# Performance work log

Measured on AMD Instinct MI355X. Metric: run time of the kernel, lower is better.

The kernel has to match this reference:

```python
import jax, jax.numpy as jnp
import numpy as np

N = 10000        # nodes
E = 160000       # edges (before self-loops)
NFEAT = 256
NHID = 128
H = 4            # heads
NCLASS = 40
NLAYERS = 2
DT = 1.0
ALPHA = 1.0
GAMMA = 1.0
NEG_SLOPE = 0.2  # GATConv leaky_relu slope


def setup_inputs() -> dict:
    key = jax.random.key(0)
    ks = jax.random.split(key, 12)

    def glorot(k, shape):
        fan_in, fan_out = shape[-1], shape[0]
        lim = (6.0 / (fan_in + fan_out)) ** 0.5
        return jax.random.uniform(k, shape, jnp.float32, -lim, lim)

    return {
        "x": jax.random.normal(ks[0], (N, NFEAT), jnp.float32),
        "edge_index": jax.random.randint(ks[1], (2, E), 0, N, jnp.int64),
        "enc_w": glorot(ks[2], (NHID, NFEAT)),
        "enc_b": jnp.zeros((NHID,), jnp.float32),
        "res_w": glorot(ks[3], (H * NHID, NHID)),
        "res_b": jnp.zeros((H * NHID,), jnp.float32),
        "gat_w": glorot(ks[4], (H * NHID, NHID)),
        "att_src": glorot(ks[5], (H, NHID)) * 0.1,
        "att_dst": glorot(ks[6], (H, NHID)) * 0.1,
        "gat_b": jnp.zeros((H * NHID,), jnp.float32),
        "dec_w": glorot(ks[7], (NCLASS, NHID)),
        "dec_b": jnp.zeros((NCLASS,), jnp.float32),
    }


def _gat_conv(x, src, dst, gat_w, att_src, att_dst, gat_b):
    # x: [N, NHID] -> per-head features [N, H, C]
    xh = (x @ gat_w.T).reshape(N, H, NHID)
    a_src = jnp.sum(xh * att_src[None], axis=-1)  # [N, H]
    a_dst = jnp.sum(xh * att_dst[None], axis=-1)  # [N, H]
    e = jax.nn.leaky_relu(a_src[src] + a_dst[dst], NEG_SLOPE)  # [E', H]
    # segment softmax over incoming edges of each destination node
    m = jax.ops.segment_max(e, dst, num_segments=N)            # [N, H]
    e = jnp.exp(e - m[dst])
    s = jax.ops.segment_sum(e, dst, num_segments=N)            # [N, H]
    alpha = e / s[dst]                                          # [E', H]
    msg = xh[src] * alpha[:, :, None]                           # [E', H, C]
    out = jax.ops.segment_sum(msg, dst, num_segments=N)         # [N, H, C]
    return out.reshape(N, H * NHID) + gat_b


def reference(x, edge_index, enc_w, enc_b, res_w, res_b, gat_w,
              att_src, att_dst, gat_b, dec_w, dec_b):
    # add self-loops (GATConv default)
    loop = jnp.arange(N, dtype=edge_index.dtype)
    src = jnp.concatenate([edge_index[0], loop])
    dst = jnp.concatenate([edge_index[1], loop])

    Y = jax.nn.relu(x @ enc_w.T + enc_b)  # [N, NHID]
    X = Y
    for _ in range(NLAYERS):
        conv = _gat_conv(X, src, dst, gat_w, att_src, att_dst, gat_b)  # [N, H*NHID]
        res = X @ res_w.T + res_b                                       # [N, H*NHID]
        # faithful to .view(n_nodes, -1, nheads).mean(-1): [N, NHID, H] -> mean over heads axis
        z = jax.nn.elu(conv + res).reshape(N, NHID, H).mean(axis=-1)    # [N, NHID]
        Y = Y + DT * (z - ALPHA * Y - GAMMA * X)
        X = X + DT * Y
    return X @ dec_w.T + dec_b  # [N, NCLASS]
```

## Files before the change

kernel.cpp:

```cpp
#include <hip/hip_runtime.h>
#include <math.h>

#define NN 10000
#define EE 160000
#define EP 170000
#define NFEAT 256
#define NHID 128
#define NH 4
#define HF 512
#define NCLASS 40
#define FCOLS 1088

typedef __attribute__((ext_vector_type(8))) short bf8;
typedef __attribute__((ext_vector_type(8))) unsigned short u16x8;
typedef __attribute__((ext_vector_type(4))) float f4;

__device__ __forceinline__ float leaky02(float x) { return x >= 0.0f ? x : 0.2f * x; }

__device__ __forceinline__ unsigned short f2bf(float f) {
    unsigned u = __builtin_bit_cast(unsigned, f);
    unsigned r = (u + 0x7FFF + ((u >> 16) & 1)) >> 16;
    return (unsigned short)r;
}
__device__ __forceinline__ float bf2f(unsigned short h) {
    return __builtin_bit_cast(float, (unsigned)h << 16);
}

__device__ __forceinline__ int swz(int row, int c) {
    return ((((c >> 3) ^ (row & 7)) << 3) | (c & 7));
}

__device__ __forceinline__ void gl_lds16(const unsigned short* g, unsigned short* l)
{
    __builtin_amdgcn_global_load_lds(
        (const __attribute__((address_space(1))) unsigned int*)g,
        (__attribute__((address_space(3))) unsigned int*)l, 16, 0, 0);
}

#define C_X   2560000
#define C_EW  (C_X + 32768)
#define C_FW  (C_EW + 131072)
#define C_DW  (C_FW + 5120)
#define CVT_B  1333
#define ATTW_B (CVT_B + 8)
#define TOT_B  (ATTW_B + 166)

__global__ __launch_bounds__(256)
void fused0_k(const float* __restrict__ x, const float* __restrict__ enc_w,
              const float* __restrict__ gat_w, const float* __restrict__ res_w,
              const float* __restrict__ dec_w,
              const float* __restrict__ att_src, const float* __restrict__ att_dst,
              const float* __restrict__ res_b, const float* __restrict__ gat_b,
              const int* __restrict__ ei,
              unsigned short* __restrict__ xhi, unsigned short* __restrict__ ewhi,
              unsigned short* __restrict__ fwhi, unsigned short* __restrict__ dwhi,
              float* __restrict__ biasRG, int* __restrict__ cnt)
{
    int bId = blockIdx.x;
    int t = threadIdx.x;
    if (bId < CVT_B) {
        int iu = bId * 256 + t;
        int i = iu * 8;
        if (i >= C_DW) return;
        const float* src = nullptr; unsigned short* ph; int j, row, c, Kd;
        if (i < C_X)       { j = i;        src = x;     ph = xhi;
                             row = j >> 8; c = j & 255; Kd = 256; }
        else if (i < C_EW) { j = i - C_X;  src = enc_w; ph = ewhi;
                             row = j >> 8; c = j & 255; Kd = 256; }
        else if (i < C_FW) { j = i - C_EW; ph = fwhi;
                             row = j >> 7; c = j & 127; Kd = 128; }
        else               { j = i - C_FW; src = dec_w; ph = dwhi;
                             row = j >> 7; c = j & 127; Kd = 128; }
        float4 v0, v1;
        if (src) { v0 = *(const float4*)(src + j); v1 = *(const float4*)(src + j + 4); }
        else {
            const float* s2 = (j < 65536) ? (gat_w + j) : (res_w + j - 65536);
            v0 = *(const float4*)s2; v1 = *(const float4*)(s2 + 4);
        }
        float vv[8] = {v0.x, v0.y, v0.z, v0.w, v1.x, v1.y, v1.z, v1.w};
        unsigned short hs[8];
#pragma unroll
        for (int k = 0; k < 8; ++k) hs[k] = f2bf(vv[k]);
        int outp = row * Kd + swz(row, c);
        *(u16x8*)(ph + outp) = *(u16x8*)hs;
    } else if (bId < ATTW_B) {
        __shared__ float sm[256];
        int b = bId - CVT_B;
        int is_dst = b >> 2, h = b & 3;
        const float* att = is_dst ? att_dst : att_src;
        int k = t & 127, half = t >> 7;
        float s = 0.0f;
#pragma unroll 4
        for (int c = half * 64; c < half * 64 + 64; ++c)
            s = fmaf(gat_w[(size_t)(h * 128 + c) * 128 + k], att[h * 128 + c], s);
        sm[t] = s;
        __syncthreads();
        if (t < 128) {
            float v = sm[t] + sm[t + 128];
            int R = 1024 + is_dst * 4 + h;
            fwhi[(size_t)R * 128 + swz(R, k)] = f2bf(v);
        }
        for (int i = b * 896 + t; i < (b + 1) * 896; i += 256)
            fwhi[1032 * 128 + i] = 0;
        if (b < 2) {
            int c = b * 256 + t;
            biasRG[c] = res_b[c] + gat_b[c];
        }
    } else {
        for (int e = (bId - ATTW_B) * 256 + t; e < EP; e += (TOT_B - ATTW_B) * 256) {
            int d = (e < EE) ? ei[EE + e] : (e - EE);
            atomicAdd(&cnt[d], 1);
        }
    }
}

template<int MODE, int KTILES, int MERGE>
__global__ __launch_bounds__(256)
void gemm3_k(const unsigned short* __restrict__ A, const unsigned short* __restrict__ B,
             const float* __restrict__ bias, float* __restrict__ outF,
             unsigned short* __restrict__ outH, unsigned short* __restrict__ outL,
             float* __restrict__ a_src, float* __restrict__ a_dst, int M,
             const int* __restrict__ ei, const int* __restrict__ cnt,
             int* __restrict__ row_ptr, int* __restrict__ cursor, int* __restrict__ csr)
{
    constexpr int K = KTILES * 128;
    __shared__ __align__(16) unsigned short smem[2 * 64 * 128];
    const int tid = threadIdx.x;

    if (MERGE && blockIdx.y == gridDim.y - 1) {
        if (MERGE == 1) {
            if (blockIdx.x != 0) return;
            int* smi = (int*)smem;
            int i0 = tid * 40, i1 = min(i0 + 40, NN);
            int part = 0;
            for (int i = i0; i < i1; ++i) part += cnt[i];
            smi[tid] = part;
            __syncthreads();
            for (int off = 1; off < 256; off <<= 1) {
                int v = (tid >= off) ? smi[tid - off] : 0;
                __syncthreads();
                smi[tid] += v;
                __syncthreads();
            }
            int run = smi[tid] - part;
            for (int i = i0; i < i1; ++i) { row_ptr[i] = run; run += cnt[i]; }
            if (tid == 255) row_ptr[NN] = run;
        } else {
            int stride = gridDim.x * 256;
            for (int e = blockIdx.x * 256 + tid; e < EP; e += stride) {
                int s, d;
                if (e < EE) { s = ei[e]; d = ei[EE + e]; } else { s = e - EE; d = s; }
                int pos = row_ptr[d] + atomicAdd(&cursor[d], 1);
                csr[pos] = s;
            }
        }
        return;
    }

    unsigned short* sA = smem;
    unsigned short* sB = smem + 8192;

    const int lane = tid & 63, wv = tid >> 6;
    const int wr = (wv >> 1) * 32, wc = (wv & 1) * 32;
    const int bm = blockIdx.x * 64, bn = blockIdx.y * 64;
    const int r16 = lane & 15, q4 = lane >> 4;

    f4 acc[2][2];
#pragma unroll
    for (int i = 0; i < 2; ++i)
#pragma unroll
        for (int j = 0; j < 2; ++j) acc[i][j] = (f4){0.f, 0.f, 0.f, 0.f};

    const int ra0 = wr + r16;
    const int rb0 = wc + r16;

    for (int kt = 0; kt < KTILES; ++kt) {
        if (kt) __syncthreads();
#pragma unroll
        for (int j = 0; j < 4; ++j) {
            int i = tid + j * 256;
            int row = i >> 4, u = i & 15;
            int arow = min(bm + row, M - 1);
            size_t ga = (size_t)arow * K + kt * 128 + u * 8;
            size_t gb = (size_t)(bn + row) * K + kt * 128 + u * 8;
            int lb = (wv * 64 + j * 256) * 8;
            gl_lds16(A + ga, sA + lb);
            gl_lds16(B + gb, sB + lb);
        }
        __syncthreads();

#pragma unroll
        for (int ks = 0; ks < 4; ++ks) {
            int u = ks * 4 + q4;
            int oa0 = ra0 * 128 + ((u ^ (ra0 & 7)) * 8);
            int ob0 = rb0 * 128 + ((u ^ (rb0 & 7)) * 8);
            int oa1 = oa0 + 16 * 128;
            int ob1 = ob0 + 16 * 128;
            bf8 A0 = *(const bf8*)(sA + oa0);
            bf8 A1 = *(const bf8*)(sA + oa1);
            bf8 B0 = *(const bf8*)(sB + ob0);
            bf8 B1 = *(const bf8*)(sB + ob1);

            acc[0][0] = __builtin_amdgcn_mfma_f32_16x16x32_bf16(A0, B0, acc[0][0], 0, 0, 0);
            acc[0][1] = __builtin_amdgcn_mfma_f32_16x16x32_bf16(A0, B1, acc[0][1], 0, 0, 0);
            acc[1][0] = __builtin_amdgcn_mfma_f32_16x16x32_bf16(A1, B0, acc[1][0], 0, 0, 0);
            acc[1][1] = __builtin_amdgcn_mfma_f32_16x16x32_bf16(A1, B1, acc[1][1], 0, 0, 0);
        }
    }

    const int rbase = q4 * 4;

    if (MODE == 0 || (MODE == 2 && bn >= 1024)) {
#pragma unroll
        for (int i = 0; i < 2; ++i)
#pragma unroll
            for (int j = 0; j < 2; ++j)
#pragma unroll
                for (int r = 0; r < 4; ++r) {
                    int row = bm + wr + i * 16 + rbase + r;
                    int col = bn + wc + j * 16 + r16;
                    if (row >= M) continue;
                    float v = acc[i][j][r];
                    if (MODE == 0) {
                        if (col < NCLASS)
                            outF[(size_t)row * NCLASS + col] = v + bias[col];
                    } else {
                        if (col < 1032) {
                            int h = col - 1024;
                            if (h < 4) a_src[row * 4 + h] = v;
                            else       a_dst[row * 4 + h - 4] = v;
                        }
                    }
                }
        return;
    }

    __syncthreads();
    float* sC = (float*)smem;
#pragma unroll
    for (int i = 0; i < 2; ++i)
#pragma unroll
        for (int j = 0; j < 2; ++j)
#pragma unroll
            for (int r = 0; r < 4; ++r)
                sC[(wr + i * 16 + rbase + r) * 65 + (wc + j * 16 + r16)] = acc[i][j][r];
    __syncthreads();

    int row = tid >> 2, seg = tid & 3, c0 = seg * 16;
    int grow = bm + row;
    if (grow < M) {
        float v[16];
#pragma unroll
        for (int k = 0; k < 16; ++k) v[k] = sC[row * 65 + c0 + k];

        if (MODE == 1) {
            unsigned short hs[16];
#pragma unroll
            for (int k = 0; k < 16; ++k)
                hs[k] = f2bf(fmaxf(v[k] + bias[bn + c0 + k], 0.0f));
#pragma unroll
            for (int uu = 0; uu < 2; ++uu) {
                int ug = (bn + c0) / 8 + uu;
                int pu = ug ^ (grow & 7);
                *(u16x8*)(outH + (size_t)grow * 128 + pu * 8) = *(u16x8*)(hs + uu * 8);
            }
        } else {
            if (bn < 512) {
                unsigned short hs[16];
#pragma unroll
                for (int k = 0; k < 16; ++k) hs[k] = f2bf(v[k]);
                *(u16x8*)(outH + (size_t)grow * 512 + bn + c0)     = *(u16x8*)hs;
                *(u16x8*)(outH + (size_t)grow * 512 + bn + c0 + 8) = *(u16x8*)(hs + 8);
            } else {
                unsigned short hs[16];
#pragma unroll
                for (int k = 0; k < 16; ++k) hs[k] = f2bf(v[k] + bias[bn - 512 + c0 + k]);
                *(u16x8*)(outL + (size_t)grow * 512 + (bn - 512) + c0)     = *(u16x8*)hs;
                *(u16x8*)(outL + (size_t)grow * 512 + (bn - 512) + c0 + 8) = *(u16x8*)(hs + 8);
            }
        }
    }
}

__global__ __launch_bounds__(256)
void agg_k(const int* __restrict__ row_ptr, const int* __restrict__ csr,
           const float* __restrict__ a_src, const float* __restrict__ a_dst,
           const unsigned short* __restrict__ xh_b, const unsigned short* __restrict__ resb,
           unsigned short* __restrict__ Xhi)
{
    int bx = blockIdx.x;
    int h  = bx / 2500;
    int ng = bx - h * 2500;
    int wv = threadIdx.x >> 6, lane = threadIdx.x & 63;
    int d = ng * 4 + wv;
    int beg = row_ptr[d], end = row_ptr[d + 1];
    int eg = lane >> 4, c16 = lane & 15;
    int cb = h * 128 + c16 * 8;
    float ad = a_dst[d * 4 + h];
    u16x8 rv = *(const u16x8*)(resb + (size_t)d * HF + cb);

    float acc[8];
#pragma unroll
    for (int k = 0; k < 8; ++k) acc[k] = 0.0f;
    float ssum = 0.0f;

    int e = beg;
    for (; e + 16 <= end; e += 16) {
        int sv[4]; float w[4]; u16x8 v[4];
#pragma unroll
        for (int q = 0; q < 4; ++q) sv[q] = csr[e + q * 4 + eg];
#pragma unroll
        for (int q = 0; q < 4; ++q) v[q] = *(const u16x8*)(xh_b + (size_t)sv[q] * HF + cb);
#pragma unroll
        for (int q = 0; q < 4; ++q) {
            w[q] = __expf(leaky02(a_src[sv[q] * 4 + h] + ad));
            ssum += w[q];
        }
#pragma unroll
        for (int q = 0; q < 4; ++q)
#pragma unroll
            for (int k = 0; k < 8; ++k) acc[k] = fmaf(w[q], bf2f(v[q][k]), acc[k]);
    }
    for (; e + 4 <= end; e += 4) {
        int s = csr[e + eg];
        u16x8 v = *(const u16x8*)(xh_b + (size_t)s * HF + cb);
        float w = __expf(leaky02(a_src[s * 4 + h] + ad));
        ssum += w;
#pragma unroll
        for (int k = 0; k < 8; ++k) acc[k] = fmaf(w, bf2f(v[k]), acc[k]);
    }
    if (e + eg < end) {
        int s = csr[e + eg];
        u16x8 v = *(const u16x8*)(xh_b + (size_t)s * HF + cb);
        float w = __expf(leaky02(a_src[s * 4 + h] + ad));
        ssum += w;
#pragma unroll
        for (int k = 0; k < 8; ++k) acc[k] = fmaf(w, bf2f(v[k]), acc[k]);
    }

#pragma unroll
    for (int off = 16; off <= 32; off <<= 1) {
        ssum += __shfl_xor(ssum, off);
#pragma unroll
        for (int k = 0; k < 8; ++k) acc[k] += __shfl_xor(acc[k], off);
    }

    float inv = 1.0f / ssum;
    float uv[8];
#pragma unroll
    for (int k = 0; k < 8; ++k) {
        float v = fmaf(acc[k], inv, bf2f(rv[k]));
        uv[k] = (v > 0.0f) ? v : expm1f(v);
    }
    float z0 = (uv[0] + uv[1] + uv[2] + uv[3]) * 0.25f;
    float z1 = (uv[4] + uv[5] + uv[6] + uv[7]) * 0.25f;
    if (eg == 0) {
        int col = h * 32 + c16 * 2;
        unsigned short h0b = f2bf(z0), h1b = f2bf(z1);
        size_t idx = (size_t)d * NHID + swz(d, col);
        *(unsigned*)(Xhi + idx) = ((unsigned)h1b << 16) | h0b;
    }
}

extern "C" void kernel_launch(void* const* d_in, const int* in_sizes, int n_in,
                              void* d_out, int out_size, void* d_ws, size_t ws_size,
                              hipStream_t stream)
{
    const float* x       = (const float*)d_in[0];
    const int*   ei      = (const int*)d_in[1];
    const float* enc_w   = (const float*)d_in[2];
    const float* enc_b   = (const float*)d_in[3];
    const float* res_w   = (const float*)d_in[4];
    const float* res_b   = (const float*)d_in[5];
    const float* gat_w   = (const float*)d_in[6];
    const float* att_src = (const float*)d_in[7];
    const float* att_dst = (const float*)d_in[8];
    const float* gat_b   = (const float*)d_in[9];
    const float* dec_w   = (const float*)d_in[10];
    const float* dec_b   = (const float*)d_in[11];
    float* out = (float*)d_out;

    char* p = (char*)d_ws;
    auto alloc = [&](size_t bytes) -> void* {
        void* r = (void*)p;
        p += (bytes + 255) & ~(size_t)255;
        return r;
    };
    float* a_src  = (float*)alloc(40000 * 4);
    float* a_dst  = (float*)alloc(40000 * 4);
    float* biasRG = (float*)alloc(512 * 4);
    unsigned short* xh_b = (unsigned short*)alloc(5120000 * 2);
    unsigned short* resb = (unsigned short*)alloc(5120000 * 2);
    unsigned short* Xhi  = (unsigned short*)alloc(1280000 * 2);
    unsigned short* xhi  = (unsigned short*)alloc(2560000 * 2);
    unsigned short* ewhi = (unsigned short*)alloc(32768 * 2);
    unsigned short* fwhi = (unsigned short*)alloc(FCOLS * 128 * 2);
    int* row_ptr = (int*)alloc(10004 * 4);
    int* csr     = (int*)alloc(170000 * 4);
    char* zbase = p;
    unsigned short* dwhi = (unsigned short*)alloc(8192 * 2);
    int* cnt    = (int*)alloc(10000 * 4);
    int* cursor = (int*)alloc(10000 * 4);
    size_t zbytes = (size_t)(p - zbase);

    hipMemsetAsync(zbase, 0, zbytes, stream);

    fused0_k<<<TOT_B, 256, 0, stream>>>(
        x, enc_w, gat_w, res_w, dec_w, att_src, att_dst, res_b, gat_b, ei,
        xhi, ewhi, fwhi, dwhi, biasRG, cnt);

    gemm3_k<1, 2, 1><<<dim3(157, 3), 256, 0, stream>>>(
        xhi, ewhi, enc_b, nullptr, Xhi, nullptr, nullptr, nullptr, NN,
        nullptr, cnt, row_ptr, nullptr, nullptr);

    gemm3_k<2, 1, 2><<<dim3(157, 18), 256, 0, stream>>>(
        Xhi, fwhi, biasRG, nullptr, xh_b, resb, a_src, a_dst, NN,
        ei, nullptr, row_ptr, cursor, csr);
    agg_k<<<10000, 256, 0, stream>>>(row_ptr, csr, a_src, a_dst, xh_b, resb, Xhi);

    gemm3_k<2, 1, 0><<<dim3(157, 17), 256, 0, stream>>>(
        Xhi, fwhi, biasRG, nullptr, xh_b, resb, a_src, a_dst, NN,
        nullptr, nullptr, nullptr, nullptr, nullptr);
    agg_k<<<10000, 256, 0, stream>>>(row_ptr, csr, a_src, a_dst, xh_b, resb, Xhi);

    gemm3_k<0, 1, 0><<<dim3(157, 1), 256, 0, stream>>>(
        Xhi, dwhi, dec_b, out, nullptr, nullptr, nullptr, nullptr, NN,
        nullptr, nullptr, nullptr, nullptr, nullptr);
}
```

Before: 206.7 us.

## Fuse decoder projection into final aggregation kernel via per-head atomic partial sums

Drops the separate decoder GEMM launch and the bf16 conversion of dec_w. The last aggregation kernel now stages each block's z values in shared memory and computes its 32-column slice of the 40-class projection. Each head-block adds its partial into the fp32 output with atomics, so the output must be zeroed by an added memset. This removes one kernel launch and a re-read of X. In exchange it adds 4 atomics per output element, fp32 scalar FMAs in place of MFMA, and a block-level sync in the aggregation kernel.

```diff
diff --git a/kernel.cpp b/kernel.cpp
--- a/kernel.cpp
+++ b/kernel.cpp
@@ -40,20 +40,18 @@
 #define C_X   2560000
 #define C_EW  (C_X + 32768)
 #define C_FW  (C_EW + 131072)
-#define C_DW  (C_FW + 5120)
-#define CVT_B  1333
+#define CVT_B  1330
 #define ATTW_B (CVT_B + 8)
 #define TOT_B  (ATTW_B + 166)
 
 __global__ __launch_bounds__(256)
 void fused0_k(const float* __restrict__ x, const float* __restrict__ enc_w,
               const float* __restrict__ gat_w, const float* __restrict__ res_w,
-              const float* __restrict__ dec_w,
               const float* __restrict__ att_src, const float* __restrict__ att_dst,
               const float* __restrict__ res_b, const float* __restrict__ gat_b,
               const int* __restrict__ ei,
               unsigned short* __restrict__ xhi, unsigned short* __restrict__ ewhi,
-              unsigned short* __restrict__ fwhi, unsigned short* __restrict__ dwhi,
+              unsigned short* __restrict__ fwhi,
               float* __restrict__ biasRG, int* __restrict__ cnt)
 {
     int bId = blockIdx.x;
@@ -61,15 +59,12 @@
     if (bId < CVT_B) {
         int iu = bId * 256 + t;
         int i = iu * 8;
-        if (i >= C_DW) return;
         const float* src = nullptr; unsigned short* ph; int j, row, c, Kd;
         if (i < C_X)       { j = i;        src = x;     ph = xhi;
                              row = j >> 8; c = j & 255; Kd = 256; }
         else if (i < C_EW) { j = i - C_X;  src = enc_w; ph = ewhi;
                              row = j >> 8; c = j & 255; Kd = 256; }
-        else if (i < C_FW) { j = i - C_EW; ph = fwhi;
-                             row = j >> 7; c = j & 127; Kd = 128; }
-        else               { j = i - C_FW; src = dec_w; ph = dwhi;
+        else               { j = i - C_EW; ph = fwhi;
                              row = j >> 7; c = j & 127; Kd = 128; }
         float4 v0, v1;
         if (src) { v0 = *(const float4*)(src + j); v1 = *(const float4*)(src + j + 4); }
@@ -117,7 +112,7 @@
 template<int MODE, int KTILES, int MERGE>
 __global__ __launch_bounds__(256)
 void gemm3_k(const unsigned short* __restrict__ A, const unsigned short* __restrict__ B,
-             const float* __restrict__ bias, float* __restrict__ outF,
+             const float* __restrict__ bias,
              unsigned short* __restrict__ outH, unsigned short* __restrict__ outL,
              float* __restrict__ a_src, float* __restrict__ a_dst, int M,
              const int* __restrict__ ei, const int* __restrict__ cnt,
@@ -210,7 +205,7 @@
 
     const int rbase = q4 * 4;
 
-    if (MODE == 0 || (MODE == 2 && bn >= 1024)) {
+    if (MODE == 2 && bn >= 1024) {
 #pragma unroll
         for (int i = 0; i < 2; ++i)
 #pragma unroll
@@ -219,18 +214,11 @@
                 for (int r = 0; r < 4; ++r) {
                     int row = bm + wr + i * 16 + rbase + r;
                     int col = bn + wc + j * 16 + r16;
-                    if (row >= M) continue;
+                    if (row >= M || col >= 1032) continue;
                     float v = acc[i][j][r];
-                    if (MODE == 0) {
-                        if (col < NCLASS)
-                            outF[(size_t)row * NCLASS + col] = v + bias[col];
-                    } else {
-                        if (col < 1032) {
-                            int h = col - 1024;
-                            if (h < 4) a_src[row * 4 + h] = v;
-                            else       a_dst[row * 4 + h - 4] = v;
-                        }
-                    }
+                    int h = col - 1024;
+                    if (h < 4) a_src[row * 4 + h] = v;
+                    else       a_dst[row * 4 + h - 4] = v;
                 }
         return;
     }
@@ -282,12 +270,16 @@
     }
 }
 
+template<int DEC>
 __global__ __launch_bounds__(256)
 void agg_k(const int* __restrict__ row_ptr, const int* __restrict__ csr,
            const float* __restrict__ a_src, const float* __restrict__ a_dst,
            const unsigned short* __restrict__ xh_b, const unsigned short* __restrict__ resb,
-           unsigned short* __restrict__ Xhi)
+           unsigned short* __restrict__ Xhi,
+           const float* __restrict__ dec_w, const float* __restrict__ dec_b,
+           float* __restrict__ out)
 {
+    __shared__ float zbuf[4][32];
     int bx = blockIdx.x;
     int h  = bx / 2500;
     int ng = bx - h * 2500;
@@ -359,6 +351,23 @@
         unsigned short h0b = f2bf(z0), h1b = f2bf(z1);
         size_t idx = (size_t)d * NHID + swz(d, col);
         *(unsigned*)(Xhi + idx) = ((unsigned)h1b << 16) | h0b;
+        if (DEC) {
+            zbuf[wv][c16 * 2]     = z0;
+            zbuf[wv][c16 * 2 + 1] = z1;
+        }
+    }
+
+    if (DEC) {
+        __syncthreads();
+        int t = threadIdx.x;
+        if (t < 160) {
+            int nd = t / 40, cp = t - nd * 40;
+            float s = (h == 0) ? dec_b[cp] : 0.0f;
+            const float* wr = dec_w + cp * 128 + h * 32;
+#pragma unroll 8
+            for (int c = 0; c < 32; ++c) s = fmaf(zbuf[nd][c], wr[c], s);
+            atomicAdd(&out[(size_t)(ng * 4 + nd) * NCLASS + cp], s);
+        }
     }
 }
 
@@ -398,32 +407,30 @@
     int* row_ptr = (int*)alloc(10004 * 4);
     int* csr     = (int*)alloc(170000 * 4);
     char* zbase = p;
-    unsigned short* dwhi = (unsigned short*)alloc(8192 * 2);
     int* cnt    = (int*)alloc(10000 * 4);
     int* cursor = (int*)alloc(10000 * 4);
     size_t zbytes = (size_t)(p - zbase);
 
     hipMemsetAsync(zbase, 0, zbytes, stream);
+    hipMemsetAsync(out, 0, (size_t)NN * NCLASS * sizeof(float), stream);
 
     fused0_k<<<TOT_B, 256, 0, stream>>>(
-        x, enc_w, gat_w, res_w, dec_w, att_src, att_dst, res_b, gat_b, ei,
-        xhi, ewhi, fwhi, dwhi, biasRG, cnt);
+        x, enc_w, gat_w, res_w, att_src, att_dst, res_b, gat_b, ei,
+        xhi, ewhi, fwhi, biasRG, cnt);
 
     gemm3_k<1, 2, 1><<<dim3(157, 3), 256, 0, stream>>>(
-        xhi, ewhi, enc_b, nullptr, Xhi, nullptr, nullptr, nullptr, NN,
+        xhi, ewhi, enc_b, Xhi, nullptr, nullptr, nullptr, NN,
         nullptr, cnt, row_ptr, nullptr, nullptr);
 
     gemm3_k<2, 1, 2><<<dim3(157, 18), 256, 0, stream>>>(
-        Xhi, fwhi, biasRG, nullptr, xh_b, resb, a_src, a_dst, NN,
+        Xhi, fwhi, biasRG, xh_b, resb, a_src, a_dst, NN,
         ei, nullptr, row_ptr, cursor, csr);
-    agg_k<<<10000, 256, 0, stream>>>(row_ptr, csr, a_src, a_dst, xh_b, resb, Xhi);
+    agg_k<0><<<10000, 256, 0, stream>>>(row_ptr, csr, a_src, a_dst, xh_b, resb, Xhi,
+                                        nullptr, nullptr, nullptr);
 
     gemm3_k<2, 1, 0><<<dim3(157, 17), 256, 0, stream>>>(
-        Xhi, fwhi, biasRG, nullptr, xh_b, resb, a_src, a_dst, NN,
+        Xhi, fwhi, biasRG, xh_b, resb, a_src, a_dst, NN,
         nullptr, nullptr, nullptr, nullptr, nullptr);
-    agg_k<<<10000, 256, 0, stream>>>(row_ptr, csr, a_src, a_dst, xh_b, resb, Xhi);
-
-    gemm3_k<0, 1, 0><<<dim3(157, 1), 256, 0, stream>>>(
-        Xhi, dwhi, dec_b, out, nullptr, nullptr, nullptr, nullptr, NN,
-        nullptr, nullptr, nullptr, nullptr, nullptr);
-}
+    agg_k<1><<<10000, 256, 0, stream>>>(row_ptr, csr, a_src, a_dst, xh_b, resb, Xhi,
+                                        dec_w, dec_b, out);
+}
```

Result: slower. 221.3 us (+7.1%).
